# Kernel tuning notes

Measured on AMD Instinct MI355X. Metric: run time of the kernel, lower is better.

## Reference

```python
import jax, jax.numpy as jnp
import numpy as np
from jax import lax

AB = 2            # activation quant bits (args.ab)
BN_EPS = 1e-4


def binarize(w):
    # DoReFa 1-bit weight: sign(w) with straight-through estimator
    wb = jnp.where(w >= 0, 1.0, -1.0).astype(w.dtype)
    return w + lax.stop_gradient(wb - w)


def quantize(x, bits):
    # uniform quantization of x in [0,1] to `bits` bits, STE backward
    n = float(2 ** bits - 1)
    q = jnp.round(x * n) / n
    return x + lax.stop_gradient(q - x)


def conv(x, w, pad, b=None):
    y = lax.conv_general_dilated(x, w, window_strides=(1, 1),
                                 padding=[(pad, pad), (pad, pad)],
                                 dimension_numbers=('NCHW', 'OIHW', 'NCHW'))
    if b is not None:
        y = y + b[None, :, None, None]
    return y


def maxpool2(x):
    return lax.reduce_window(x, -jnp.inf, lax.max, (1, 1, 2, 2), (1, 1, 2, 2), 'VALID')


def bn(x, gamma, beta, mean, var):
    inv = gamma * lax.rsqrt(var + BN_EPS)
    return (x - mean[None, :, None, None]) * inv[None, :, None, None] + beta[None, :, None, None]


def setup_inputs() -> dict:
    key = jax.random.key(0)
    ks = jax.random.split(key, 16)
    s = lambda k, shape, sc=0.1: jax.random.normal(k, shape, dtype=jnp.float32) * sc
    return {
        'x': jax.random.uniform(ks[0], (4096, 1, 28, 28), dtype=jnp.float32),
        'w1': s(ks[1], (64, 1, 3, 3)), 'b1': s(ks[2], (64,)),
        'w2': s(ks[3], (64, 64, 3, 3)),
        'g1': 1.0 + s(ks[4], (64,)), 'be1': s(ks[5], (64,)),
        'm1': s(ks[6], (64,)), 'v1': 0.5 + jax.random.uniform(ks[7], (64,), dtype=jnp.float32),
        'w3': s(ks[8], (64, 64, 3, 3)),
        'g2': 1.0 + s(ks[9], (64,)), 'be2': s(ks[10], (64,)),
        'm2': s(ks[11], (64,)), 'v2': 0.5 + jax.random.uniform(ks[12], (64,), dtype=jnp.float32),
        'fw1': s(ks[13], (512, 1600)), 'fb1': s(ks[13], (512,)),
        'fw2': s(ks[14], (10, 512)), 'fb2': s(ks[15], (10,)),
    }


def reference(x, w1, b1, w2, g1, be1, m1, v1, w3, g2, be2, m2, v2, fw1, fb1, fw2, fb2):
    x = x.reshape(-1, 1, 28, 28)
    # features
    h = conv(x, binarize(w1), pad=1, b=b1)                 # [B,64,28,28]
    h = maxpool2(h)                                        # [B,64,14,14]
    h = quantize(jnp.clip(h, 0.0, 1.0), AB)
    h = conv(h, binarize(w2), pad=1)                       # [B,64,14,14]
    h = bn(h, g1, be1, m1, v1)
    h = quantize(jnp.clip(h, 0.0, 1.0), AB)
    h = maxpool2(h)                                        # [B,64,7,7]
    h = conv(h, binarize(w3), pad=0)                       # [B,64,5,5]
    h = bn(h, g2, be2, m2, v2)
    h = quantize(jnp.clip(h, 0.0, 1.0), AB)
    # NCHW -> NHWC -> flatten (matches permute((0,2,3,1)) + view)
    h = jnp.transpose(h, (0, 2, 3, 1)).reshape(-1, 64 * 5 * 5)
    # classifier
    h = h @ binarize(fw1).T + fb1                          # [B,512]
    h = h @ fw2.T + fb2                                    # [B,10]
    return jax.nn.log_softmax(h, axis=-1)
```

## Files before the change

### kernel.cpp

```cpp
#include <hip/hip_runtime.h>

#define DEV __device__ __forceinline__

typedef int v4i __attribute__((ext_vector_type(4)));
typedef short v8s __attribute__((ext_vector_type(8)));
typedef float v4f __attribute__((ext_vector_type(4)));
typedef unsigned long long u64;

DEV unsigned int quant3(float y3) {
    return (unsigned int)(int)rintf(fminf(fmaxf(y3, 0.f), 3.f));
}

DEV int imax(int a, int b) { return a > b ? a : b; }
DEV int imin(int a, int b) { return a < b ? a : b; }

DEV unsigned int f2bf(float x) {
    union { float f; unsigned u; } v; v.f = x;
    unsigned r = v.u + 0x7fffu + ((v.u >> 16) & 1u);
    return r >> 16;
}
DEV float bf2f(unsigned int b) {
    union { unsigned u; float f; } v; v.u = b << 16;
    return v.f;
}
#define SPLIT3(v, H, M, L)                        \
    unsigned int H = f2bf(v);                     \
    float r1_##H = (v) - bf2f(H);                 \
    unsigned int M = f2bf(r1_##H);                \
    unsigned int L = f2bf(r1_##H - bf2f(M));

DEV v8s mk_v8s(u64 a, u64 b) {
    union { u64 q[2]; v8s s; } u; u.q[0] = a; u.q[1] = b; return u.s;
}

DEV int chpos(int c) { return (c & 15) * 4 + (c >> 4); }

__global__ __launch_bounds__(256, 8) void k_conv1_mfma(
    const float* __restrict__ x, const float* __restrict__ w1f,
    const float* __restrict__ b1, unsigned char* __restrict__ a1,
    const float* __restrict__ w2, const float* __restrict__ w3,
    const float* __restrict__ fw1,
    char* __restrict__ w2p, char* __restrict__ w3p, char* __restrict__ fw1s) {
    __shared__ u64 simg[960];
    __shared__ float sxf[960];
    int b = blockIdx.x, tid = threadIdx.x;
    for (int i = tid; i < 960; i += 256) {
        int y = i >> 5, xc = i & 31;
        float v = 0.f;
        if (y >= 1 && y <= 28 && xc >= 1 && xc <= 28)
            v = x[(size_t)b * 784 + (y - 1) * 28 + (xc - 1)];
        sxf[i] = v;
        SPLIT3(v, h, m, lo);
        simg[i] = (u64)(h | (m << 16)) | ((u64)lo << 32);
    }
    int l = tid & 63, lr = l & 15, lg = l >> 4, w = tid >> 6;
    int t0 = lg * 2, t1 = t0 + 1;
    int ky0 = (t0 * 21846) >> 16, kx0 = t0 - ky0 * 3;
    int ky1 = (t1 * 21846) >> 16, kx1 = t1 - ky1 * 3;
    int dt0 = (ky0 * 32 + kx0) * 8, dt1 = (ky1 * 32 + kx1) * 8;
    v8s bf[4];
    float s8[4], b3[4];
#pragma unroll
    for (int nt = 0; nt < 4; ++nt) {
        const float* wr = w1f + (nt * 16 + lr) * 9;
        unsigned sa = (wr[t0] >= 0.f) ? 0x3F80u : 0xBF80u;
        unsigned sb = (wr[t1] >= 0.f) ? 0x3F80u : 0xBF80u;
        union { unsigned d[4]; v8s s; } u;
        u.d[0] = sa | (sa << 16); u.d[1] = sa;
        u.d[2] = sb | (sb << 16); u.d[3] = sb;
        bf[nt] = u.s;
        s8[nt] = (wr[8] >= 0.f) ? 1.f : -1.f;
        b3[nt] = 3.f * b1[nt * 16 + lr];
    }
    __syncthreads();

    const unsigned char* sib = (const unsigned char*)simg;
    unsigned char* outb = a1 + (size_t)b * 12544;
    for (int mt = w; mt < 49; mt += 4) {
        int s = mt * 4 + (lr >> 2);
        int qy = (s * 4682) >> 16;
        int qx = s - qy * 14;
        int cy = 2 * qy + ((lr >> 1) & 1);
        int cx = 2 * qx + (lr & 1);
        int base = (cy * 32 + cx) * 8;
        u64 qa = *(const u64*)(sib + base + dt0);
        u64 qb = *(const u64*)(sib + base + dt1);
        v8s af = mk_v8s(qa, qb);
        v4f a0 = {0.f, 0.f, 0.f, 0.f}, a1v = {0.f, 0.f, 0.f, 0.f};
        v4f a2v = {0.f, 0.f, 0.f, 0.f}, a3v = {0.f, 0.f, 0.f, 0.f};
        a0  = __builtin_amdgcn_mfma_f32_16x16x32_bf16(af, bf[0], a0, 0, 0, 0);
        a1v = __builtin_amdgcn_mfma_f32_16x16x32_bf16(af, bf[1], a1v, 0, 0, 0);
        a2v = __builtin_amdgcn_mfma_f32_16x16x32_bf16(af, bf[2], a2v, 0, 0, 0);
        a3v = __builtin_amdgcn_mfma_f32_16x16x32_bf16(af, bf[3], a3v, 0, 0, 0);
        int q = mt * 4 + lg;
        int Qy = (q * 4682) >> 16;
        int Qx = q - Qy * 14;
        const float* xr = &sxf[(2 * Qy + 2) * 32 + (2 * Qx + 2)];
        float x8_0 = xr[0], x8_1 = xr[1], x8_2 = xr[32], x8_3 = xr[33];
        unsigned dw;
        {
            float m0 = fmaxf(fmaxf(fmaf(s8[0], x8_0, a0[0]),  fmaf(s8[0], x8_1, a0[1])),
                             fmaxf(fmaf(s8[0], x8_2, a0[2]),  fmaf(s8[0], x8_3, a0[3])));
            float m1 = fmaxf(fmaxf(fmaf(s8[1], x8_0, a1v[0]), fmaf(s8[1], x8_1, a1v[1])),
                             fmaxf(fmaf(s8[1], x8_2, a1v[2]), fmaf(s8[1], x8_3, a1v[3])));
            float m2 = fmaxf(fmaxf(fmaf(s8[2], x8_0, a2v[0]), fmaf(s8[2], x8_1, a2v[1])),
                             fmaxf(fmaf(s8[2], x8_2, a2v[2]), fmaf(s8[2], x8_3, a2v[3])));
            float m3 = fmaxf(fmaxf(fmaf(s8[3], x8_0, a3v[0]), fmaf(s8[3], x8_1, a3v[1])),
                             fmaxf(fmaf(s8[3], x8_2, a3v[2]), fmaf(s8[3], x8_3, a3v[3])));
            dw  = quant3(fmaf(m0, 3.f, b3[0]));
            dw |= quant3(fmaf(m1, 3.f, b3[1])) << 8;
            dw |= quant3(fmaf(m2, 3.f, b3[2])) << 16;
            dw |= quant3(fmaf(m3, 3.f, b3[3])) << 24;
        }
        *(unsigned*)(outb + q * 64 + lr * 4) = dw;
    }

    {
        int i = b * 256 + tid;
        if (i < 36864) {
            int co = i / 576, r = i - co * 576;
            int ci = r / 9, t = r - ci * 9;
            int p = chpos(ci);
            int off = t * 4096 + (p >> 4) * 1024 + co * 16 + (p & 15);
            w2p[off] = (w2[i] >= 0.f) ? 1 : -1;
            w3p[off] = (w3[i] >= 0.f) ? 1 : -1;
        }
        if (i < 819200) {
            int o = i / 1600, r2 = i - o * 1600;
            int pix = r2 >> 6, ch = r2 & 63;
            fw1s[o * 1600 + pix * 64 + chpos(ch)] = (fw1[i] >= 0.f) ? 1 : -1;
        }
    }
}

__global__ __launch_bounds__(512, 4) void k_conv2_mfma(
    const unsigned char* __restrict__ a1, const char* __restrict__ w2p,
    const float* __restrict__ g1, const float* __restrict__ be1,
    const float* __restrict__ m1, const float* __restrict__ v1,
    unsigned char* __restrict__ a2) {
    __shared__ unsigned char sa[2 * 16384];
    __shared__ char sw[36864];
    int b0 = blockIdx.x * 2, tid = threadIdx.x;
    if (tid < 480) {
        int imz = (tid >= 240) ? 1 : 0;
        int t2 = tid - imz * 240;
        int ck = t2 & 3, e = t2 >> 2;
        int py, px;
        if (e < 16)      { py = 0;      px = e; }
        else if (e < 32) { py = 15;     px = e - 16; }
        else if (e < 46) { py = e - 31; px = 0; }
        else             { py = e - 45; px = 15; }
        *(uint4*)(sa + imz * 16384 + ck * 4096 + (py * 16 + px) * 16) =
            make_uint4(0, 0, 0, 0);
    }
    {
        const uint4* src = (const uint4*)(a1 + (size_t)b0 * 12544);
        for (int i = tid; i < 1568; i += 512) {
            int im = i / 784, r = i - im * 784;
            int ck = r / 196, pixel = r - ck * 196;
            int py = pixel / 14, px = pixel - py * 14;
            *(uint4*)(sa + im * 16384 + ck * 4096 + ((py + 1) * 16 + px + 1) * 16) =
                src[im * 784 + pixel * 4 + ck];
        }
        const uint4* wsrc = (const uint4*)w2p;
        uint4* wdst = (uint4*)sw;
        for (int i = tid; i < 2304; i += 512) wdst[i] = wsrc[i];
    }
    __syncthreads();

    int w8 = tid >> 6, l = tid & 63;
    int img = w8 >> 2, w = w8 & 3;
    int lr = l & 15, lg = l >> 4;
    const unsigned char* sai = sa + img * 16384;
    int abase[4], mts[4];
#pragma unroll
    for (int j = 0; j < 4; ++j) {
        int mt = w + 4 * j;
        mts[j] = mt;
        int s = mt * 4 + (lr >> 2);
        if (s > 48) s = 48;
        int qy = s / 7, qx = s - qy * 7;
        int ty = 2 * qy + ((lr >> 1) & 1);
        int tx = 2 * qx + (lr & 1);
        abase[j] = lg * 4096 + (ty * 16 + tx) * 16;
    }
    v4i acc[4][4] = {};
#pragma unroll
    for (int t = 0; t < 9; ++t) {
        int ky = t / 3, kx = t - ky * 3;
        int boff = t * 4096 + lg * 1024 + lr * 16;
        v4i bfw[4];
#pragma unroll
        for (int nt = 0; nt < 4; ++nt)
            bfw[nt] = *(const v4i*)(sw + boff + nt * 256);
        int aoff = (ky * 16 + kx) * 16;
#pragma unroll
        for (int j = 0; j < 4; ++j) {
            if (mts[j] < 13) {
                v4i af = *(const v4i*)(sai + abase[j] + aoff);
#pragma unroll
                for (int nt = 0; nt < 4; ++nt)
                    acc[j][nt] = __builtin_amdgcn_mfma_i32_16x16x64_i8(
                        af, bfw[nt], acc[j][nt], 0, 0, 0);
            }
        }
    }

    float sc4[4], of4[4];
#pragma unroll
    for (int nt = 0; nt < 4; ++nt) {
        int ch = nt * 16 + lr;
        float si = g1[ch] * rsqrtf(v1[ch] + 1e-4f);
        sc4[nt] = si;
        of4[nt] = 3.f * (be1[ch] - m1[ch] * si);
    }
#pragma unroll
    for (int j = 0; j < 4; ++j) {
        int q = mts[j] * 4 + lg;
        if (q < 49) {
            unsigned dw = 0;
#pragma unroll
            for (int nt = 0; nt < 4; ++nt) {
                int mx = imax(imax(acc[j][nt][0], acc[j][nt][1]),
                              imax(acc[j][nt][2], acc[j][nt][3]));
                int mn = imin(imin(acc[j][nt][0], acc[j][nt][1]),
                              imin(acc[j][nt][2], acc[j][nt][3]));
                float sc = sc4[nt];
                int v = (sc >= 0.f) ? mx : mn;
                dw |= quant3(fmaf((float)v, sc, of4[nt])) << (8 * nt);
            }
            *(unsigned*)(a2 + (size_t)(b0 + img) * 3136 + q * 64 + lr * 4) = dw;
        }
    }
}

__global__ __launch_bounds__(256, 2) void k_conv3_mfma(
    const unsigned char* __restrict__ a2, const char* __restrict__ w3p,
    const float* __restrict__ g2, const float* __restrict__ be2,
    const float* __restrict__ m2, const float* __restrict__ v2,
    unsigned char* __restrict__ a3) {
    __shared__ unsigned char sa[4 * 3136];
    __shared__ char sw[36864];
    __shared__ unsigned char so[4 * 2560];
    int b0 = blockIdx.x * 4, tid = threadIdx.x;
    {
        const uint4* src = (const uint4*)(a2 + (size_t)b0 * 3136);
        for (int i = tid; i < 784; i += 256) {
            int img = i / 196, r = i - img * 196;
            int ck = r / 49, pixel = r - ck * 49;
            *(uint4*)(sa + img * 3136 + ck * 784 + pixel * 16) =
                src[img * 196 + pixel * 4 + ck];
        }
        const uint4* wsrc = (const uint4*)w3p;
        uint4* wdst = (uint4*)sw;
        for (int i = tid; i < 2304; i += 256) wdst[i] = wsrc[i];
    }
    __syncthreads();

    int w = tid >> 6, l = tid & 63;
    int lr = l & 15, lg = l >> 4;
    const unsigned char* sai = sa + w * 3136;
    int abase[2];
#pragma unroll
    for (int mt = 0; mt < 2; ++mt) {
        int p = mt * 16 + lr;
        if (p > 24) p = 24;
        int oy = p / 5, ox = p - oy * 5;
        abase[mt] = lg * 784 + (oy * 7 + ox) * 16;
    }
    v4i acc[2][4] = {};
#pragma unroll
    for (int t = 0; t < 9; ++t) {
        int ky = t / 3, kx = t - ky * 3;
        int boff = t * 4096 + lg * 1024 + lr * 16;
        v4i bfw[4];
#pragma unroll
        for (int nt = 0; nt < 4; ++nt)
            bfw[nt] = *(const v4i*)(sw + boff + nt * 256);
        int aoff = (ky * 7 + kx) * 16;
#pragma unroll
        for (int mt = 0; mt < 2; ++mt) {
            v4i af = *(const v4i*)(sai + abase[mt] + aoff);
#pragma unroll
            for (int nt = 0; nt < 4; ++nt)
                acc[mt][nt] = __builtin_amdgcn_mfma_i32_16x16x64_i8(
                    af, bfw[nt], acc[mt][nt], 0, 0, 0);
        }
    }

    float sc4[4], of4[4];
#pragma unroll
    for (int nt = 0; nt < 4; ++nt) {
        int ch = nt * 16 + lr;
        float si = g2[ch] * rsqrtf(v2[ch] + 1e-4f);
        sc4[nt] = si;
        of4[nt] = 3.f * (be2[ch] - m2[ch] * si);
    }
    unsigned char* soi = so + w * 2560;
#pragma unroll
    for (int mt = 0; mt < 2; ++mt)
#pragma unroll
        for (int r = 0; r < 4; ++r) {
            int pixel = mt * 16 + lg * 4 + r;
            unsigned dw = 0;
#pragma unroll
            for (int nt = 0; nt < 4; ++nt)
                dw |= quant3(fmaf((float)acc[mt][nt][r], sc4[nt], of4[nt])) << (8 * nt);
            *(unsigned*)(soi + pixel * 80 + lr * 4) = dw;
        }
    __syncthreads();
    for (int idx = tid; idx < 400; idx += 256) {
        int img = idx / 100, r = idx - img * 100;
        int p = r >> 2, c0 = r & 3;
        *(uint4*)(a3 + (size_t)(b0 + img) * 1600 + r * 16) =
            *(const uint4*)(so + img * 2560 + p * 80 + c0 * 16);
    }
}

__global__ __launch_bounds__(256, 8) void k_fc1_mfma(
    const unsigned char* __restrict__ a3, const char* __restrict__ fw1s,
    const float* __restrict__ fb1, float* __restrict__ h1) {
    __shared__ unsigned char sA[64 * 80];
    __shared__ unsigned char sB[32 * 80];
    __shared__ float sbias[32];
    int bb = (blockIdx.x >> 4) * 64;
    int ob = (blockIdx.x & 15) * 32;
    int tid = threadIdx.x;
    int row = tid >> 2, seg = tid & 3;
    if (tid < 32) sbias[tid] = fb1[ob + tid];
    const unsigned char* Ag = a3 + (size_t)(bb + row) * 1600 + seg * 16;
    const char* Bg = fw1s + (size_t)(ob + (row & 31)) * 1600 + seg * 16;
    uint4 av = *(const uint4*)Ag;
    uint4 bv = make_uint4(0, 0, 0, 0);
    if (tid < 128) bv = *(const uint4*)Bg;

    int w = tid >> 6, l = tid & 63;
    int wm = w >> 1, wn = w & 1;
    int lr = l & 15, lg = l >> 4;
    const unsigned char* sAr = sA + (wm * 32 + lr) * 80 + lg * 16;
    const unsigned char* sBr = sB + (wn * 16 + lr) * 80 + lg * 16;
    v4i acc[2] = {};

    for (int k0 = 0; k0 < 1600; k0 += 64) {
        *(uint4*)(sA + row * 80 + seg * 16) = av;
        if (tid < 128) *(uint4*)(sB + row * 80 + seg * 16) = bv;
        __syncthreads();
        if (k0 < 1536) {
            av = *(const uint4*)(Ag + k0 + 64);
            if (tid < 128) bv = *(const uint4*)(Bg + k0 + 64);
        }
        v4i af0 = *(const v4i*)(sAr);
        v4i af1 = *(const v4i*)(sAr + 16 * 80);
        v4i bf0 = *(const v4i*)(sBr);
        acc[0] = __builtin_amdgcn_mfma_i32_16x16x64_i8(af0, bf0, acc[0], 0, 0, 0);
        acc[1] = __builtin_amdgcn_mfma_i32_16x16x64_i8(af1, bf0, acc[1], 0, 0, 0);
        __syncthreads();
    }

    const float inv3 = 1.f / 3.f;
    int gcol = ob + wn * 16 + lr;
    float bias = sbias[wn * 16 + lr];
#pragma unroll
    for (int mt = 0; mt < 2; ++mt)
#pragma unroll
        for (int r = 0; r < 4; ++r) {
            int grow = bb + wm * 32 + mt * 16 + lg * 4 + r;
            h1[(size_t)grow * 512 + gcol] = (float)acc[mt][r] * inv3 + bias;
        }
}

__global__ __launch_bounds__(256) void k_fc2(
    const float* __restrict__ h1, const float* __restrict__ fw2,
    const float* __restrict__ fb2, float* __restrict__ out) {
    __shared__ float sw[5120];
    __shared__ float sb[16];
    int tid = threadIdx.x;
    for (int i = tid; i < 5120; i += 256) sw[i] = fw2[i];
    if (tid < 10) sb[tid] = fb2[tid];
    __syncthreads();

    int wv = tid >> 6, lane = tid & 63;
    int b = blockIdx.x * 4 + wv;
    const float* hr = h1 + (size_t)b * 512;
    float p[10];
#pragma unroll
    for (int o = 0; o < 10; ++o) p[o] = 0.f;
    for (int k = lane; k < 512; k += 64) {
        float hv = hr[k];
#pragma unroll
        for (int o = 0; o < 10; ++o) p[o] += hv * sw[o * 512 + k];
    }
#pragma unroll
    for (int o = 0; o < 10; ++o) {
#pragma unroll
        for (int off = 32; off > 0; off >>= 1) p[o] += __shfl_xor(p[o], off, 64);
        p[o] += sb[o];
    }
    float mx = p[0];
#pragma unroll
    for (int o = 1; o < 10; ++o) mx = fmaxf(mx, p[o]);
    float se = 0.f;
#pragma unroll
    for (int o = 0; o < 10; ++o) se += expf(p[o] - mx);
    float lse = logf(se) + mx;
    float myv = 0.f;
#pragma unroll
    for (int o = 0; o < 10; ++o) myv = (lane == o) ? p[o] : myv;
    if (lane < 10) out[(size_t)b * 10 + lane] = myv - lse;
}

extern "C" void kernel_launch(void* const* d_in, const int* in_sizes, int n_in,
                              void* d_out, int out_size, void* d_ws, size_t ws_size,
                              hipStream_t stream) {
    const float* x   = (const float*)d_in[0];
    const float* w1  = (const float*)d_in[1];
    const float* b1  = (const float*)d_in[2];
    const float* w2  = (const float*)d_in[3];
    const float* g1  = (const float*)d_in[4];
    const float* be1 = (const float*)d_in[5];
    const float* m1  = (const float*)d_in[6];
    const float* v1  = (const float*)d_in[7];
    const float* w3  = (const float*)d_in[8];
    const float* g2  = (const float*)d_in[9];
    const float* be2 = (const float*)d_in[10];
    const float* m2  = (const float*)d_in[11];
    const float* v2  = (const float*)d_in[12];
    const float* fw1 = (const float*)d_in[13];
    const float* fb1 = (const float*)d_in[14];
    const float* fw2 = (const float*)d_in[15];
    const float* fb2 = (const float*)d_in[16];
    float* out = (float*)d_out;

    char* ws = (char*)d_ws;
    char* w2p  = ws;
    char* w3p  = ws + 36864;
    char* fw1s = ws + 73728;
    unsigned char* a1 = (unsigned char*)(ws + 892928);
    unsigned char* a2 = a1 + 51380224;
    unsigned char* a3 = a2 + 12845056;
    float* h1 = (float*)(void*)a1;

    k_conv1_mfma<<<4096, 256, 0, stream>>>(x, w1, b1, a1, w2, w3, fw1,
                                           w2p, w3p, fw1s);
    k_conv2_mfma<<<2048, 512, 0, stream>>>(a1, w2p, g1, be1, m1, v1, a2);
    k_conv3_mfma<<<1024, 256, 0, stream>>>(a2, w3p, g2, be2, m2, v2, a3);
    k_fc1_mfma<<<1024, 256, 0, stream>>>(a3, fw1s, fb1, h1);
    k_fc2<<<1024, 256, 0, stream>>>(h1, fw2, fb2, out);
}
```

Baseline: 99.33 us.

## Read conv2/conv3 activation fragments directly from global memory instead of LDS staging

Removes the shared-memory staging of input activations (including the zero-padded halo) in the conv2 and conv3 MFMA kernels. Each lane now loads its 16-byte A fragment straight from global memory and applies bounds masking for padding in conv2. This cuts LDS footprint and the staging barrier, and conv3's launch bound now requests 4 blocks instead of 2. The cost is repeated, less coalesced global and L2 reads of the same activations across the 9 taps.

```diff
diff --git a/kernel.cpp b/kernel.cpp
--- a/kernel.cpp
+++ b/kernel.cpp
@@ -138,30 +138,9 @@
     const float* __restrict__ g1, const float* __restrict__ be1,
     const float* __restrict__ m1, const float* __restrict__ v1,
     unsigned char* __restrict__ a2) {
-    __shared__ unsigned char sa[2 * 16384];
     __shared__ char sw[36864];
     int b0 = blockIdx.x * 2, tid = threadIdx.x;
-    if (tid < 480) {
-        int imz = (tid >= 240) ? 1 : 0;
-        int t2 = tid - imz * 240;
-        int ck = t2 & 3, e = t2 >> 2;
-        int py, px;
-        if (e < 16)      { py = 0;      px = e; }
-        else if (e < 32) { py = 15;     px = e - 16; }
-        else if (e < 46) { py = e - 31; px = 0; }
-        else             { py = e - 45; px = 15; }
-        *(uint4*)(sa + imz * 16384 + ck * 4096 + (py * 16 + px) * 16) =
-            make_uint4(0, 0, 0, 0);
-    }
     {
-        const uint4* src = (const uint4*)(a1 + (size_t)b0 * 12544);
-        for (int i = tid; i < 1568; i += 512) {
-            int im = i / 784, r = i - im * 784;
-            int ck = r / 196, pixel = r - ck * 196;
-            int py = pixel / 14, px = pixel - py * 14;
-            *(uint4*)(sa + im * 16384 + ck * 4096 + ((py + 1) * 16 + px + 1) * 16) =
-                src[im * 784 + pixel * 4 + ck];
-        }
         const uint4* wsrc = (const uint4*)w2p;
         uint4* wdst = (uint4*)sw;
         for (int i = tid; i < 2304; i += 512) wdst[i] = wsrc[i];
@@ -171,8 +150,8 @@
     int w8 = tid >> 6, l = tid & 63;
     int img = w8 >> 2, w = w8 & 3;
     int lr = l & 15, lg = l >> 4;
-    const unsigned char* sai = sa + img * 16384;
-    int abase[4], mts[4];
+    const unsigned char* ag = a1 + (size_t)(b0 + img) * 12544 + lg * 16;
+    int ty[4], tx[4], mts[4];
 #pragma unroll
     for (int j = 0; j < 4; ++j) {
         int mt = w + 4 * j;
@@ -180,9 +159,8 @@
         int s = mt * 4 + (lr >> 2);
         if (s > 48) s = 48;
         int qy = s / 7, qx = s - qy * 7;
-        int ty = 2 * qy + ((lr >> 1) & 1);
-        int tx = 2 * qx + (lr & 1);
-        abase[j] = lg * 4096 + (ty * 16 + tx) * 16;
+        ty[j] = 2 * qy + ((lr >> 1) & 1);
+        tx[j] = 2 * qx + (lr & 1);
     }
     v4i acc[4][4] = {};
 #pragma unroll
@@ -193,11 +171,15 @@
 #pragma unroll
         for (int nt = 0; nt < 4; ++nt)
             bfw[nt] = *(const v4i*)(sw + boff + nt * 256);
-        int aoff = (ky * 16 + kx) * 16;
 #pragma unroll
         for (int j = 0; j < 4; ++j) {
             if (mts[j] < 13) {
-                v4i af = *(const v4i*)(sai + abase[j] + aoff);
+                int iy = ty[j] + ky - 1;
+                int ix = tx[j] + kx - 1;
+                bool ok = ((unsigned)iy < 14u) & ((unsigned)ix < 14u);
+                int pix = ok ? (iy * 14 + ix) : 0;
+                v4i af = *(const v4i*)(ag + pix * 64);
+                if (!ok) { af[0] = 0; af[1] = 0; af[2] = 0; af[3] = 0; }
 #pragma unroll
                 for (int nt = 0; nt < 4; ++nt)
                     acc[j][nt] = __builtin_amdgcn_mfma_i32_16x16x64_i8(
@@ -234,23 +216,15 @@
     }
 }
 
-__global__ __launch_bounds__(256, 2) void k_conv3_mfma(
+__global__ __launch_bounds__(256, 4) void k_conv3_mfma(
     const unsigned char* __restrict__ a2, const char* __restrict__ w3p,
     const float* __restrict__ g2, const float* __restrict__ be2,
     const float* __restrict__ m2, const float* __restrict__ v2,
     unsigned char* __restrict__ a3) {
-    __shared__ unsigned char sa[4 * 3136];
     __shared__ char sw[36864];
     __shared__ unsigned char so[4 * 2560];
     int b0 = blockIdx.x * 4, tid = threadIdx.x;
     {
-        const uint4* src = (const uint4*)(a2 + (size_t)b0 * 3136);
-        for (int i = tid; i < 784; i += 256) {
-            int img = i / 196, r = i - img * 196;
-            int ck = r / 49, pixel = r - ck * 49;
-            *(uint4*)(sa + img * 3136 + ck * 784 + pixel * 16) =
-                src[img * 196 + pixel * 4 + ck];
-        }
         const uint4* wsrc = (const uint4*)w3p;
         uint4* wdst = (uint4*)sw;
         for (int i = tid; i < 2304; i += 256) wdst[i] = wsrc[i];
@@ -259,14 +233,14 @@
 
     int w = tid >> 6, l = tid & 63;
     int lr = l & 15, lg = l >> 4;
-    const unsigned char* sai = sa + w * 3136;
-    int abase[2];
+    const unsigned char* ag = a2 + (size_t)(b0 + w) * 3136 + lg * 16;
+    int oy[2], ox[2];
 #pragma unroll
     for (int mt = 0; mt < 2; ++mt) {
         int p = mt * 16 + lr;
         if (p > 24) p = 24;
-        int oy = p / 5, ox = p - oy * 5;
-        abase[mt] = lg * 784 + (oy * 7 + ox) * 16;
+        oy[mt] = p / 5;
+        ox[mt] = p - oy[mt] * 5;
     }
     v4i acc[2][4] = {};
 #pragma unroll
@@ -277,10 +251,10 @@
 #pragma unroll
         for (int nt = 0; nt < 4; ++nt)
             bfw[nt] = *(const v4i*)(sw + boff + nt * 256);
-        int aoff = (ky * 7 + kx) * 16;
 #pragma unroll
         for (int mt = 0; mt < 2; ++mt) {
-            v4i af = *(const v4i*)(sai + abase[mt] + aoff);
+            int pix = (oy[mt] + ky) * 7 + ox[mt] + kx;
+            v4i af = *(const v4i*)(ag + pix * 64);
 #pragma unroll
             for (int nt = 0; nt < 4; ++nt)
                 acc[mt][nt] = __builtin_amdgcn_mfma_i32_16x16x64_i8(
```

New measurement: 123.3 us. +24.1%, slower.

## Process more images per block in conv2/conv3 to amortize weight staging

Applied to the files above, without the earlier changes.

conv2 now handles 3 images per 768-thread block using a compact shared layout that stacks the images vertically and shares padding rows between them, with clamped loads and guarded stores for the tail. conv3 handles 8 images per 512-thread block and writes results straight to global memory, dropping the shared staging buffer and its second barrier. The aim is to spread the fixed per-block cost of copying weights into shared memory over more images and to shrink the shared footprint per image. In exchange, blocks get larger, conv2 does redundant tail work, and conv3 stores are narrower and less coalesced.

```diff
diff --git a/kernel.cpp b/kernel.cpp
--- a/kernel.cpp
+++ b/kernel.cpp
@@ -133,45 +133,40 @@
     }
 }
 
-__global__ __launch_bounds__(512, 4) void k_conv2_mfma(
+__global__ __launch_bounds__(768, 6) void k_conv2_mfma(
     const unsigned char* __restrict__ a1, const char* __restrict__ w2p,
     const float* __restrict__ g1, const float* __restrict__ be1,
     const float* __restrict__ m1, const float* __restrict__ v1,
     unsigned char* __restrict__ a2) {
-    __shared__ unsigned char sa[2 * 16384];
+    __shared__ unsigned char sa[44176];
     __shared__ char sw[36864];
-    int b0 = blockIdx.x * 2, tid = threadIdx.x;
-    if (tid < 480) {
-        int imz = (tid >= 240) ? 1 : 0;
-        int t2 = tid - imz * 240;
-        int ck = t2 & 3, e = t2 >> 2;
-        int py, px;
-        if (e < 16)      { py = 0;      px = e; }
-        else if (e < 32) { py = 15;     px = e - 16; }
-        else if (e < 46) { py = e - 31; px = 0; }
-        else             { py = e - 45; px = 15; }
-        *(uint4*)(sa + imz * 16384 + ck * 4096 + (py * 16 + px) * 16) =
-            make_uint4(0, 0, 0, 0);
-    }
+    int b0 = blockIdx.x * 3, tid = threadIdx.x;
+    if (tid < 408) {
+        int ck = tid / 102, e = tid - ck * 102;
+        int row, col;
+        if (e < 60) { int pr = e / 15; row = pr * 15; col = e - pr * 15; }
+        else        { int d = e - 60; row = d + 1 + (d / 14); col = 0; }
+        *(uint4*)(sa + ck * 11040 + (row * 15 + col) * 16) = make_uint4(0, 0, 0, 0);
+    }
+    if (tid == 408) *(uint4*)(sa + 44160) = make_uint4(0, 0, 0, 0);
     {
-        const uint4* src = (const uint4*)(a1 + (size_t)b0 * 12544);
-        for (int i = tid; i < 1568; i += 512) {
+        for (int i = tid; i < 2352; i += 768) {
             int im = i / 784, r = i - im * 784;
             int ck = r / 196, pixel = r - ck * 196;
             int py = pixel / 14, px = pixel - py * 14;
-            *(uint4*)(sa + im * 16384 + ck * 4096 + ((py + 1) * 16 + px + 1) * 16) =
-                src[im * 784 + pixel * 4 + ck];
+            size_t img_g = b0 + im; if (img_g > 4095) img_g = 4095;
+            *(uint4*)(sa + ck * 11040 + ((15 * im + 1 + py) * 15 + 1 + px) * 16) =
+                *(const uint4*)(a1 + img_g * 12544 + (size_t)(pixel * 4 + ck) * 16);
         }
         const uint4* wsrc = (const uint4*)w2p;
         uint4* wdst = (uint4*)sw;
-        for (int i = tid; i < 2304; i += 512) wdst[i] = wsrc[i];
+        for (int i = tid; i < 2304; i += 768) wdst[i] = wsrc[i];
     }
     __syncthreads();
 
-    int w8 = tid >> 6, l = tid & 63;
-    int img = w8 >> 2, w = w8 & 3;
+    int w12 = tid >> 6, l = tid & 63;
+    int img = w12 >> 2, w = w12 & 3;
     int lr = l & 15, lg = l >> 4;
-    const unsigned char* sai = sa + img * 16384;
     int abase[4], mts[4];
 #pragma unroll
     for (int j = 0; j < 4; ++j) {
@@ -182,7 +177,7 @@
         int qy = s / 7, qx = s - qy * 7;
         int ty = 2 * qy + ((lr >> 1) & 1);
         int tx = 2 * qx + (lr & 1);
-        abase[j] = lg * 4096 + (ty * 16 + tx) * 16;
+        abase[j] = lg * 11040 + ((15 * img + ty) * 15 + tx) * 16;
     }
     v4i acc[4][4] = {};
 #pragma unroll
@@ -193,11 +188,11 @@
 #pragma unroll
         for (int nt = 0; nt < 4; ++nt)
             bfw[nt] = *(const v4i*)(sw + boff + nt * 256);
-        int aoff = (ky * 16 + kx) * 16;
+        int aoff = (ky * 15 + kx) * 16;
 #pragma unroll
         for (int j = 0; j < 4; ++j) {
             if (mts[j] < 13) {
-                v4i af = *(const v4i*)(sai + abase[j] + aoff);
+                v4i af = *(const v4i*)(sa + abase[j] + aoff);
 #pragma unroll
                 for (int nt = 0; nt < 4; ++nt)
                     acc[j][nt] = __builtin_amdgcn_mfma_i32_16x16x64_i8(
@@ -214,38 +209,39 @@
         sc4[nt] = si;
         of4[nt] = 3.f * (be1[ch] - m1[ch] * si);
     }
-#pragma unroll
-    for (int j = 0; j < 4; ++j) {
-        int q = mts[j] * 4 + lg;
-        if (q < 49) {
-            unsigned dw = 0;
-#pragma unroll
-            for (int nt = 0; nt < 4; ++nt) {
-                int mx = imax(imax(acc[j][nt][0], acc[j][nt][1]),
-                              imax(acc[j][nt][2], acc[j][nt][3]));
-                int mn = imin(imin(acc[j][nt][0], acc[j][nt][1]),
-                              imin(acc[j][nt][2], acc[j][nt][3]));
-                float sc = sc4[nt];
-                int v = (sc >= 0.f) ? mx : mn;
-                dw |= quant3(fmaf((float)v, sc, of4[nt])) << (8 * nt);
+    if (b0 + img < 4096) {
+#pragma unroll
+        for (int j = 0; j < 4; ++j) {
+            int q = mts[j] * 4 + lg;
+            if (q < 49) {
+                unsigned dw = 0;
+#pragma unroll
+                for (int nt = 0; nt < 4; ++nt) {
+                    int mx = imax(imax(acc[j][nt][0], acc[j][nt][1]),
+                                  imax(acc[j][nt][2], acc[j][nt][3]));
+                    int mn = imin(imin(acc[j][nt][0], acc[j][nt][1]),
+                                  imin(acc[j][nt][2], acc[j][nt][3]));
+                    float sc = sc4[nt];
+                    int v = (sc >= 0.f) ? mx : mn;
+                    dw |= quant3(fmaf((float)v, sc, of4[nt])) << (8 * nt);
+                }
+                *(unsigned*)(a2 + (size_t)(b0 + img) * 3136 + q * 64 + lr * 4) = dw;
             }
-            *(unsigned*)(a2 + (size_t)(b0 + img) * 3136 + q * 64 + lr * 4) = dw;
-        }
-    }
-}
-
-__global__ __launch_bounds__(256, 2) void k_conv3_mfma(
+        }
+    }
+}
+
+__global__ __launch_bounds__(512, 4) void k_conv3_mfma(
     const unsigned char* __restrict__ a2, const char* __restrict__ w3p,
     const float* __restrict__ g2, const float* __restrict__ be2,
     const float* __restrict__ m2, const float* __restrict__ v2,
     unsigned char* __restrict__ a3) {
-    __shared__ unsigned char sa[4 * 3136];
+    __shared__ unsigned char sa[8 * 3136];
     __shared__ char sw[36864];
-    __shared__ unsigned char so[4 * 2560];
-    int b0 = blockIdx.x * 4, tid = threadIdx.x;
+    int b0 = blockIdx.x * 8, tid = threadIdx.x;
     {
         const uint4* src = (const uint4*)(a2 + (size_t)b0 * 3136);
-        for (int i = tid; i < 784; i += 256) {
+        for (int i = tid; i < 1568; i += 512) {
             int img = i / 196, r = i - img * 196;
             int ck = r / 49, pixel = r - ck * 49;
             *(uint4*)(sa + img * 3136 + ck * 784 + pixel * 16) =
@@ -253,7 +249,7 @@
         }
         const uint4* wsrc = (const uint4*)w3p;
         uint4* wdst = (uint4*)sw;
-        for (int i = tid; i < 2304; i += 256) wdst[i] = wsrc[i];
+        for (int i = tid; i < 2304; i += 512) wdst[i] = wsrc[i];
     }
     __syncthreads();
 
@@ -296,25 +292,20 @@
         sc4[nt] = si;
         of4[nt] = 3.f * (be2[ch] - m2[ch] * si);
     }
-    unsigned char* soi = so + w * 2560;
+    unsigned char* outb = a3 + (size_t)(b0 + w) * 1600;
 #pragma unroll
     for (int mt = 0; mt < 2; ++mt)
 #pragma unroll
         for (int r = 0; r < 4; ++r) {
             int pixel = mt * 16 + lg * 4 + r;
-            unsigned dw = 0;
-#pragma unroll
-            for (int nt = 0; nt < 4; ++nt)
-                dw |= quant3(fmaf((float)acc[mt][nt][r], sc4[nt], of4[nt])) << (8 * nt);
-            *(unsigned*)(soi + pixel * 80 + lr * 4) = dw;
-        }
-    __syncthreads();
-    for (int idx = tid; idx < 400; idx += 256) {
-        int img = idx / 100, r = idx - img * 100;
-        int p = r >> 2, c0 = r & 3;
-        *(uint4*)(a3 + (size_t)(b0 + img) * 1600 + r * 16) =
-            *(const uint4*)(so + img * 2560 + p * 80 + c0 * 16);
-    }
+            if (pixel < 25) {
+                unsigned dw = 0;
+#pragma unroll
+                for (int nt = 0; nt < 4; ++nt)
+                    dw |= quant3(fmaf((float)acc[mt][nt][r], sc4[nt], of4[nt])) << (8 * nt);
+                *(unsigned*)(outb + pixel * 64 + lr * 4) = dw;
+            }
+        }
 }
 
 __global__ __launch_bounds__(256, 8) void k_fc1_mfma(
@@ -442,8 +433,8 @@
 
     k_conv1_mfma<<<4096, 256, 0, stream>>>(x, w1, b1, a1, w2, w3, fw1,
                                            w2p, w3p, fw1s);
-    k_conv2_mfma<<<2048, 512, 0, stream>>>(a1, w2p, g1, be1, m1, v1, a2);
-    k_conv3_mfma<<<1024, 256, 0, stream>>>(a2, w3p, g2, be2, m2, v2, a3);
+    k_conv2_mfma<<<1366, 768, 0, stream>>>(a1, w2p, g1, be1, m1, v1, a2);
+    k_conv3_mfma<<<512, 512, 0, stream>>>(a2, w3p, g2, be2, m2, v2, a3);
     k_fc1_mfma<<<1024, 256, 0, stream>>>(a3, fw1s, fb1, h1);
     k_fc2<<<1024, 256, 0, stream>>>(h1, fw2, fb2, out);
 }
```

Result: slower. 153.2 us (+54.2%).
